# Kernel tuning notes

Measured on AMD Instinct MI355X. Metric: run time of the kernel, lower is better.

Reference implementation:

```python
import jax, jax.numpy as jnp
import numpy as np

INPUT_SIZE = 416
NUM_CLASSES = 80
A = 3  # anchors per yolo layer
SS = [13, 26, 52]  # grid sizes (strides 32/16/8)
ANCHORS = [[(116, 90), (156, 198), (373, 326)],
           [(30, 61), (62, 45), (59, 119)],
           [(10, 13), (16, 30), (33, 23)]]
B, L = 16, 50


def _build_priors():
    boxes, cols, rows, pws, phs, szs = [], [], [], [], [], []
    for l, S in enumerate(SS):
        for i in range(S):
            for j in range(S):
                cx, cy = (j + 0.5) / S, (i + 0.5) / S
                for (aw, ah) in ANCHORS[l]:
                    w, h = aw / INPUT_SIZE, ah / INPUT_SIZE
                    boxes.append((cx - 0.5 * w, cy - 0.5 * h, w, h))
                    cols.append(j); rows.append(i)
                    pws.append(aw); phs.append(ah); szs.append(S)
    f = lambda a: np.asarray(a, np.float32)
    return f(boxes), f(cols), f(rows), f(pws), f(phs), f(szs)

PRIORS_NP, PCOL_NP, PROW_NP, PPW_NP, PPH_NP, PS_NP = _build_priors()
N = PRIORS_NP.shape[0]  # 10647
OFF = np.concatenate([[0], np.cumsum([S * S * A for S in SS])])


def setup_inputs() -> dict:
    key = jax.random.key(0)
    ks = jax.random.split(key, 8)
    inp = {}
    for l, S in enumerate(SS):
        inp[f"yolo_out{l}"] = jax.random.normal(ks[l], (B, A * (NUM_CLASSES + 5), S, S), jnp.float32)
    cls = jax.random.randint(ks[3], (B, L), 0, NUM_CLASSES).astype(jnp.float32)
    valid = jax.random.uniform(ks[4], (B, L)) < 0.4
    cls = jnp.where(valid, cls, -1.0)  # class < 0 means padding label
    xy = jax.random.uniform(ks[5], (B, L, 2), minval=0.0, maxval=0.7)
    wh = jax.random.uniform(ks[6], (B, L, 2), minval=0.05, maxval=0.3)
    inp["labels"] = jnp.concatenate([cls[..., None], xy, wh], axis=-1)[:, None]  # [B,1,L,5]
    return inp


def _bce(p, t):
    # torch BCELoss (mean) with the same log clamp at -100
    lg = lambda x: jnp.maximum(jnp.log(x), -100.0)
    return jnp.mean(-(t * lg(p) + (1.0 - t) * lg(1.0 - p)))


def _build_targets(labels):
    pri = jnp.asarray(PRIORS_NP)
    lab = labels[:, 0]  # [B,L,5]
    cls = lab[..., 0]
    valid = cls >= 0.0  # [B,L]
    bx, by, bw, bh = lab[..., 1], lab[..., 2], lab[..., 3], lab[..., 4]
    px, py, pw, ph = pri[:, 0], pri[:, 1], pri[:, 2], pri[:, 3]
    # IoU of every label against every prior: [B,L,N]
    ix = jnp.maximum(px, bx[..., None]); iy = jnp.maximum(py, by[..., None])
    ax = jnp.minimum(px + pw, (bx + bw)[..., None]); ay = jnp.minimum(py + ph, (by + bh)[..., None])
    inter = jnp.maximum(ax - ix, 0.0) * jnp.maximum(ay - iy, 0.0)
    ious = inter / (pw * ph + (bw * bh)[..., None] - inter)

    # priors with IoU>=0.5 to any gt are ignored for objectness (unless chosen as best)
    suppressed = jnp.any((ious >= 0.5) & valid[..., None], axis=1)  # [B,N]

    # best prior per label; on ties, pick the middle tied index (as the original)
    m = jnp.max(ious, axis=-1, keepdims=True)
    tie = ious == m
    k = tie.sum(-1)
    rank = (k - 1) // 2 + 1
    cs = jnp.cumsum(tie, -1)
    idx = jnp.argmax(tie & (cs == rank[..., None]), axis=-1)  # [B,L]

    colc = jnp.asarray(PCOL_NP)[idx]; rowc = jnp.asarray(PROW_NP)[idx]
    pwc = jnp.asarray(PPW_NP)[idx]; phc = jnp.asarray(PPH_NP)[idx]
    Sc = jnp.asarray(PS_NP)[idx]
    dx = jnp.clip((bx + 0.5 * bw) * Sc - colc, 1e-6, 0.999999)
    dy = jnp.clip((by + 0.5 * bh) * Sc - rowc, 1e-6, 0.999999)
    t_all = jnp.stack([jnp.log(dx / (1.0 - dx)), jnp.log(dy / (1.0 - dy)),
                       jnp.log(bw * INPUT_SIZE / pwc), jnp.log(bh * INPUT_SIZE / phc)], -1)  # [B,L,4]

    flat = (jnp.arange(B)[:, None] * N + idx).reshape(-1)  # [B*L]
    vflat = valid.reshape(-1)
    g = jnp.arange(B * L)
    winner = jax.ops.segment_max(jnp.where(vflat, g, -1), flat, num_segments=B * N)
    chosen = winner >= 0  # [B*N]
    coord_t = jnp.where(chosen[:, None], t_all.reshape(-1, 4)[jnp.clip(winner, 0)], 0.0)

    cls_i = jnp.where(vflat, cls.reshape(-1).astype(jnp.int32), 0)
    class_t = jnp.zeros((B * N, NUM_CLASSES), jnp.float32).at[flat, cls_i].max(vflat.astype(jnp.float32))

    obj_t = chosen.astype(jnp.float32).reshape(B, N)
    obj_m = (chosen.reshape(B, N) | ~suppressed).astype(jnp.float32)
    pos_m = chosen.astype(jnp.float32).reshape(B, N)
    return jax.lax.stop_gradient(
        (obj_t, obj_m, pos_m, coord_t.reshape(B, N, 4), class_t.reshape(B, N, NUM_CLASSES)))


def reference(yolo_out0, yolo_out1, yolo_out2, labels):
    obj_t, obj_m, pos_m, coord_t, class_t = _build_targets(labels)
    outs = [yolo_out0, yolo_out1, yolo_out2]
    Cp5 = NUM_CLASSES + 5
    obj_loss = coord_loss = class_loss = 0.0
    for l, S in enumerate(SS):
        n0, n1 = int(OFF[l]), int(OFF[l + 1])
        out = outs[l]
        # per-prior ordering within a layer is (row, col, anchor)
        om = obj_m[:, n0:n1].reshape(B, S, S, A).transpose(0, 3, 1, 2)
        ot = obj_t[:, n0:n1].reshape(B, S, S, A).transpose(0, 3, 1, 2)
        pm = pos_m[:, n0:n1].reshape(B, S, S, A)
        ct = coord_t[:, n0:n1].reshape(B, S, S, A, 4).transpose(0, 3, 4, 1, 2).reshape(B, A * 4, S, S)
        cm = jnp.broadcast_to(pm[..., None], (B, S, S, A, 4)).transpose(0, 3, 4, 1, 2).reshape(B, A * 4, S, S)
        kt = class_t[:, n0:n1].reshape(B, S, S, A, NUM_CLASSES).transpose(0, 3, 4, 1, 2).reshape(B, A * NUM_CLASSES, S, S)
        km = jnp.broadcast_to(pm[..., None], (B, S, S, A, NUM_CLASSES)).transpose(0, 3, 4, 1, 2).reshape(B, A * NUM_CLASSES, S, S)
        oi = np.arange(A) * Cp5 + 4
        ci = (np.arange(A)[:, None] * Cp5 + np.arange(4)).reshape(-1)
        ki = (np.arange(A)[:, None] * Cp5 + 5 + np.arange(NUM_CLASSES)).reshape(-1)
        obj_loss = obj_loss + _bce(jax.nn.sigmoid(out[:, oi]) * om, ot * om)
        coord_loss = coord_loss + jnp.mean((out[:, ci] * cm - ct * cm) ** 2)
        class_loss = class_loss + _bce(jax.nn.sigmoid(out[:, ki]) * km, kt * km)
    return jnp.stack([obj_loss, coord_loss, class_loss])
```

## Files before the change

### kernel.cpp

```cpp
#include <hip/hip_runtime.h>

#define NPRI 10647
#define BB 16
#define LL 50
#define OBJ_BLOCKS 720
#define CHO_BLOCKS (BB * LL)
#define TOT_BLOCKS (OBJ_BLOCKS + CHO_BLOCKS)

#define SUPP_C 0.49999998509883880615234375

__device__ __constant__ double c_hw[3][3] = {
    {0.5*(116.0/416.0), 0.5*(156.0/416.0), 0.5*(373.0/416.0)},
    {0.5*( 30.0/416.0), 0.5*( 62.0/416.0), 0.5*( 59.0/416.0)},
    {0.5*( 10.0/416.0), 0.5*( 16.0/416.0), 0.5*( 33.0/416.0)}};
__device__ __constant__ double c_hh[3][3] = {
    {0.5*( 90.0/416.0), 0.5*(198.0/416.0), 0.5*(326.0/416.0)},
    {0.5*( 61.0/416.0), 0.5*( 45.0/416.0), 0.5*(119.0/416.0)},
    {0.5*( 23.0/416.0), 0.5*( 30.0/416.0), 0.5*( 23.0/416.0)}};
__device__ __constant__ float c_pwf[3][3] = {
    {(float)(116.0/416.0), (float)(156.0/416.0), (float)(373.0/416.0)},
    {(float)( 30.0/416.0), (float)( 62.0/416.0), (float)( 59.0/416.0)},
    {(float)( 10.0/416.0), (float)( 16.0/416.0), (float)( 33.0/416.0)}};
__device__ __constant__ float c_phf[3][3] = {
    {(float)( 90.0/416.0), (float)(198.0/416.0), (float)(326.0/416.0)},
    {(float)( 61.0/416.0), (float)( 45.0/416.0), (float)(119.0/416.0)},
    {(float)( 23.0/416.0), (float)( 30.0/416.0), (float)( 23.0/416.0)}};
__device__ __constant__ float c_pwph[3][3] = {
    {(float)(116.0/416.0)*(float)( 90.0/416.0), (float)(156.0/416.0)*(float)(198.0/416.0), (float)(373.0/416.0)*(float)(326.0/416.0)},
    {(float)( 30.0/416.0)*(float)( 61.0/416.0), (float)( 62.0/416.0)*(float)( 45.0/416.0), (float)( 59.0/416.0)*(float)(119.0/416.0)},
    {(float)( 10.0/416.0)*(float)( 23.0/416.0), (float)( 16.0/416.0)*(float)( 30.0/416.0), (float)( 33.0/416.0)*(float)( 23.0/416.0)}};
__device__ __constant__ float c_awf[3][3] = {{116,156,373},{30,62,59},{10,16,33}};
__device__ __constant__ float c_ahf[3][3] = {{90,198,326},{61,45,119},{23,30,23}};
__device__ __constant__ double c_wObj[3] = {1.0/8112.0, 1.0/32448.0, 1.0/129792.0};

__device__ inline void decode_prior(int n, int& level, int& S, int& ii, int& jj,
                                    int& aa, int& tb) {
    if (n < 507)        { level = 0; S = 13; int c = n / 3;            aa = n - 3*c;            jj = c % 13; ii = c / 13; tb = 0;   }
    else if (n < 2535)  { level = 1; S = 26; int nn = n - 507;  int c = nn / 3; aa = nn - 3*c; jj = c % 26; ii = c / 26; tb = 39;  }
    else                { level = 2; S = 52; int nn = n - 2535; int c = nn / 3; aa = nn - 3*c; jj = c % 52; ii = c / 52; tb = 117; }
}

__global__ __launch_bounds__(256) void assign_kernel(
    const float* __restrict__ labels, int* __restrict__ idxArr,
    float4* __restrict__ tcoord) {
    __shared__ float s_px[273], s_py[273], s_pxe[273], s_pye[273];
    __shared__ float s_iou[NPRI];
    __shared__ float s_w[4];
    __shared__ int   s_wsum[4];

    int tid = threadIdx.x, lane = tid & 63, wid = tid >> 6;
    int gi  = blockIdx.x;
    const float* lab = labels + gi * 5;
    float cls = lab[0];
    if (tid == 0) idxArr[gi] = -1;
    if (cls < 0.0f) return;

    for (int t = tid; t < 273; t += 256) {
        int level, aa, idx;
        if (t < 39)       { level = 0; aa = t / 13;           idx = t - 13 * aa; }
        else if (t < 117) { level = 1; int q = t - 39;  aa = q / 26; idx = q - 26 * aa; }
        else              { level = 2; int q = t - 117; aa = q / 52; idx = q - 52 * aa; }
        int S = (level == 0) ? 13 : (level == 1) ? 26 : 52;
        double c = ((double)idx + 0.5) / (double)S;
        float px = (float)(c - c_hw[level][aa]);
        float py = (float)(c - c_hh[level][aa]);
        s_px[t]  = px; s_pxe[t] = __fadd_rn(px, c_pwf[level][aa]);
        s_py[t]  = py; s_pye[t] = __fadd_rn(py, c_phf[level][aa]);
    }

    float bx = lab[1], by = lab[2], bw = lab[3], bh = lab[4];
    float bxe  = __fadd_rn(bx, bw), bye = __fadd_rn(by, bh);
    float bwbh = __fmul_rn(bw, bh);
    __syncthreads();

    float lmax = -3.0e38f;
    for (int n = tid; n < NPRI; n += 256) {
        int level, S, ii, jj, aa, tb;
        decode_prior(n, level, S, ii, jj, aa, tb);
        int tj = tb + aa * S + jj, ti = tb + aa * S + ii;
        float px = s_px[tj], pxe = s_pxe[tj];
        float py = s_py[ti], pye = s_pye[ti];
        float pwph = c_pwph[level][aa];
        float ix = fmaxf(px, bx), iy = fmaxf(py, by);
        float ax = fminf(pxe, bxe), ay = fminf(pye, bye);
        float iw = fmaxf(__fsub_rn(ax, ix), 0.0f);
        float ih = fmaxf(__fsub_rn(ay, iy), 0.0f);
        float inter = __fmul_rn(iw, ih);
        float denom = __fsub_rn(__fadd_rn(pwph, bwbh), inter);
        float iou = __fdiv_rn(inter, denom);
        s_iou[n] = iou;
        lmax = fmaxf(lmax, iou);
    }
    for (int d = 1; d < 64; d <<= 1) lmax = fmaxf(lmax, __shfl_xor(lmax, d));
    if (lane == 0) s_w[wid] = lmax;
    __syncthreads();
    float m = fmaxf(fmaxf(s_w[0], s_w[1]), fmaxf(s_w[2], s_w[3]));

    const int CH = 42;
    int start = tid * CH;
    int end   = min(start + CH, NPRI);
    int cnt = 0;
    for (int n = start; n < end; ++n) cnt += (s_iou[n] == m) ? 1 : 0;

    int incl = cnt;
    for (int d = 1; d < 64; d <<= 1) {
        int v = __shfl_up(incl, d);
        if (lane >= d) incl += v;
    }
    if (lane == 63) s_wsum[wid] = incl;
    __syncthreads();
    int woff = 0, k = 0;
    for (int w = 0; w < 4; ++w) { int v = s_wsum[w]; k += v; if (w < wid) woff += v; }
    int rank = (k - 1) / 2 + 1;
    int pre  = woff + incl - cnt;

    if (pre < rank && rank <= pre + cnt) {
        int r = rank - pre;
        int sel = -1;
        for (int n = start; n < end; ++n)
            if (s_iou[n] == m && --r == 0) { sel = n; break; }
        int level, S, ii, jj, aa, tb;
        decode_prior(sel, level, S, ii, jj, aa, tb);
        float Sf = (float)S, colf = (float)jj, rowf = (float)ii;
        float dx = __fsub_rn(__fmul_rn(__fadd_rn(bx, __fmul_rn(0.5f, bw)), Sf), colf);
        float dy = __fsub_rn(__fmul_rn(__fadd_rn(by, __fmul_rn(0.5f, bh)), Sf), rowf);
        dx = fminf(fmaxf(dx, 1e-6f), 0.999999f);
        dy = fminf(fmaxf(dy, 1e-6f), 0.999999f);
        float t0 = logf(__fdiv_rn(dx, __fsub_rn(1.0f, dx)));
        float t1 = logf(__fdiv_rn(dy, __fsub_rn(1.0f, dy)));
        float t2 = logf(__fdiv_rn(__fmul_rn(bw, 416.0f), c_awf[level][aa]));
        float t3 = logf(__fdiv_rn(__fmul_rn(bh, 416.0f), c_ahf[level][aa]));
        tcoord[gi] = make_float4(t0, t1, t2, t3);
        idxArr[gi] = sel;
    }
}

__global__ __launch_bounds__(256) void loss_kernel(
    const float* __restrict__ o0, const float* __restrict__ o1, const float* __restrict__ o2,
    const float* __restrict__ labels, const int* __restrict__ idxArr,
    const float4* __restrict__ tcoord,
    double* __restrict__ pObj, double* __restrict__ pCoord, double* __restrict__ pClass) {
    __shared__ float  s_pxv[52], s_pyv[52], s_pxev[52], s_pyev[52];
    __shared__ float  s_lbx[LL], s_lby[LL], s_lxe[LL], s_lye[LL], s_lar[LL];
    __shared__ int    s_lidx[LL];
    __shared__ int    s_lcnt;
    __shared__ int    s_cidx[LL];
    __shared__ float  s_ccls[LL];
    __shared__ double s_red[256];
    int tid = threadIdx.x, lane = tid & 63, wid = tid >> 6;

    if (blockIdx.x < OBJ_BLOCKS) {
        int bid = blockIdx.x;
        int level, m, chunk, S, SS2, lvloff;
        if (bid < 48)       { level = 0; m = bid;         chunk = 0;           S = 13; SS2 = 169;  lvloff = 0;    }
        else if (bid < 192) { level = 1; int q = bid-48;  m = q / 3;  chunk = q - 3*m;  S = 26; SS2 = 676;  lvloff = 507;  }
        else                { level = 2; int q = bid-192; m = q / 11; chunk = q - 11*m; S = 52; SS2 = 2704; lvloff = 2535; }
        int b  = m / 3;
        int aa = m - 3 * b;
        int pos = chunk * 256 + tid;

        if (tid < S) {
            double c = ((double)tid + 0.5) / (double)S;
            float px = (float)(c - c_hw[level][aa]);
            float py = (float)(c - c_hh[level][aa]);
            s_pxv[tid]  = px; s_pxev[tid] = __fadd_rn(px, c_pwf[level][aa]);
            s_pyv[tid]  = py; s_pyev[tid] = __fadd_rn(py, c_phf[level][aa]);
        }
        if (wid == 0) {
            float cls = -1.0f, lbx = 0, lby = 0, lbw = 0, lbh = 0; int idx = -1;
            if (lane < LL) {
                const float* lab = labels + (b * LL + lane) * 5;
                cls = lab[0]; lbx = lab[1]; lby = lab[2]; lbw = lab[3]; lbh = lab[4];
                idx = idxArr[b * LL + lane];
            }
            bool valid = (lane < LL) && (cls >= 0.0f);
            unsigned long long mask = __ballot(valid);
            if (valid) {
                int p = __popcll(mask & ((1ull << lane) - 1ull));
                s_lbx[p] = lbx;
                s_lby[p] = lby;
                s_lxe[p] = __fadd_rn(lbx, lbw);
                s_lye[p] = __fadd_rn(lby, lbh);
                s_lar[p] = __fmul_rn(lbw, lbh);
                s_lidx[p] = idx;
            }
            if (lane == 0) s_lcnt = __popcll(mask);
        }
        __syncthreads();

        double a = 0.0;
        if (pos < SS2) {
            const float* outp = (level == 0) ? o0 : ((level == 1) ? o1 : o2);
            float x = outp[((size_t)b * 255 + aa * 85 + 4) * SS2 + pos];
            int ii = pos / S, jj = pos - ii * S;
            int n  = lvloff + pos * 3 + aa;
            float px = s_pxv[jj], pxe = s_pxev[jj];
            float py = s_pyv[ii], pye = s_pyev[ii];
            float pwph = c_pwph[level][aa];
            bool supp = false, chosen = false;
            int cnt = s_lcnt;
            for (int l = 0; l < cnt; ++l) {
                chosen = chosen | (s_lidx[l] == n);
                float ix = fmaxf(px, s_lbx[l]);
                float iy = fmaxf(py, s_lby[l]);
                float ax = fminf(pxe, s_lxe[l]);
                float ay = fminf(pye, s_lye[l]);
                float iw = fmaxf(__fsub_rn(ax, ix), 0.0f);
                float ih = fmaxf(__fsub_rn(ay, iy), 0.0f);
                float inter = __fmul_rn(iw, ih);
                float denom = __fsub_rn(__fadd_rn(pwph, s_lar[l]), inter);
                supp = supp | ((double)inter >= SUPP_C * (double)denom);
            }
            if (chosen || !supp) {
                float p = 1.0f / (1.0f + expf(-x));
                float t = chosen ? 1.0f : 0.0f;
                float lp = fmaxf(logf(p), -100.0f);
                float lq = fmaxf(logf(1.0f - p), -100.0f);
                a = -(double)(t * lp + (1.0f - t) * lq) * c_wObj[level];
            }
        }
        s_red[tid] = a; __syncthreads();
        for (int s = 128; s > 0; s >>= 1) { if (tid < s) s_red[tid] += s_red[tid + s]; __syncthreads(); }
        if (tid == 0) pObj[bid] = s_red[0];
    } else {
        int gi = blockIdx.x - OBJ_BLOCKS;
        int b  = gi / LL, lsel = gi - b * LL;
        if (tid < LL) {
            s_cidx[tid] = idxArr[b * LL + tid];
            s_ccls[tid] = labels[(b * LL + tid) * 5];
        }
        __syncthreads();
        int sel = s_cidx[lsel];
        int maxl = -1;
        if (sel >= 0)
            for (int l = 0; l < LL; ++l) if (s_cidx[l] == sel) maxl = l;
        bool active = (sel >= 0) && (maxl == lsel);

        double vc = 0.0, vk = 0.0;
        if (active) {
            int level, S, ii, jj, aa, tb;
            decode_prior(sel, level, S, ii, jj, aa, tb);
            int SS2 = S * S;
            const float* outp = (level == 0) ? o0 : ((level == 1) ? o1 : o2);
            const float* base = outp + (size_t)b * 255 * SS2 + aa * 85 * SS2 + ii * S + jj;
            double wObj = c_wObj[level];
            if (tid < 4) {
                float4 ct = tcoord[gi];
                float ctk = (tid == 0) ? ct.x : (tid == 1) ? ct.y : (tid == 2) ? ct.z : ct.w;
                float x = base[tid * SS2];
                float d = __fsub_rn(x, ctk);
                vc = (double)__fmul_rn(d, d) * (wObj * 0.25);
            } else if (tid >= 5 && tid < 85) {
                int cc = tid - 5;
                float x = base[tid * SS2];
                float t = 0.0f;
                for (int l = 0; l < LL; ++l)
                    if (s_cidx[l] == sel && (int)s_ccls[l] == cc) t = 1.0f;
                float p = 1.0f / (1.0f + expf(-x));
                float lp = fmaxf(logf(p), -100.0f);
                float lq = fmaxf(logf(1.0f - p), -100.0f);
                vk = -(double)(t * lp + (1.0f - t) * lq) * (wObj * 0.0125);
            }
        }
        s_red[tid] = vc; __syncthreads();
        for (int s = 128; s > 0; s >>= 1) { if (tid < s) s_red[tid] += s_red[tid + s]; __syncthreads(); }
        if (tid == 0) pCoord[gi] = s_red[0];
        __syncthreads();
        s_red[tid] = vk; __syncthreads();
        for (int s = 128; s > 0; s >>= 1) { if (tid < s) s_red[tid] += s_red[tid + s]; __syncthreads(); }
        if (tid == 0) pClass[gi] = s_red[0];
    }
}

__global__ __launch_bounds__(256) void finalize_kernel(
    const double* __restrict__ pObj, const double* __restrict__ pCoord,
    const double* __restrict__ pClass, float* __restrict__ out) {
    int tid = threadIdx.x;
    double sO = 0.0, sC = 0.0, sK = 0.0;
    for (int i = tid; i < OBJ_BLOCKS; i += 256) sO += pObj[i];
    for (int i = tid; i < CHO_BLOCKS; i += 256) { sC += pCoord[i]; sK += pClass[i]; }
    __shared__ double r0[256], r1[256], r2[256];
    r0[tid] = sO; r1[tid] = sC; r2[tid] = sK;
    __syncthreads();
    for (int s = 128; s > 0; s >>= 1) {
        if (tid < s) { r0[tid] += r0[tid + s]; r1[tid] += r1[tid + s]; r2[tid] += r2[tid + s]; }
        __syncthreads();
    }
    if (tid == 0) { out[0] = (float)r0[0]; out[1] = (float)r1[0]; out[2] = (float)r2[0]; }
}

extern "C" void kernel_launch(void* const* d_in, const int* in_sizes, int n_in,
                              void* d_out, int out_size, void* d_ws, size_t ws_size,
                              hipStream_t stream) {
    const float* o0     = (const float*)d_in[0];
    const float* o1     = (const float*)d_in[1];
    const float* o2     = (const float*)d_in[2];
    const float* labels = (const float*)d_in[3];

    char* ws = (char*)d_ws;
    int*    idxArr = (int*)   (ws);
    float4* tcoord = (float4*)(ws + 3200);
    double* pObj   = (double*)(ws + 16000);
    double* pCoord = (double*)(ws + 21760);
    double* pClass = (double*)(ws + 28160);

    assign_kernel<<<BB * LL, 256, 0, stream>>>(labels, idxArr, tcoord);
    loss_kernel<<<TOT_BLOCKS, 256, 0, stream>>>(o0, o1, o2, labels, idxArr, tcoord,
                                                pObj, pCoord, pClass);
    finalize_kernel<<<1, 256, 0, stream>>>(pObj, pCoord, pClass, (float*)d_out);
}
```

Before: 122.3 us.

## Fuse assign, loss and finalize kernels into one cooperative kernel with grid syncs

Merges the three launches into a single cooperative kernel of 800 blocks that uses grid-wide syncs between the assignment, loss and final-reduction phases. The per-label IoU array is no longer kept in shared memory; IoU values are recomputed in the max, count and select passes so that shared memory per block shrinks and more blocks can be resident. The aim is to remove launch overhead and inter-kernel gaps, at the cost of extra IoU arithmetic, grid-sync cost, and the loss blocks doing both objectness and class work serially.

```diff
diff --git a/kernel.cpp b/kernel.cpp
--- a/kernel.cpp
+++ b/kernel.cpp
@@ -1,11 +1,14 @@
 #include <hip/hip_runtime.h>
+#include <hip/hip_cooperative_groups.h>
+
+namespace cg = cooperative_groups;
 
 #define NPRI 10647
 #define BB 16
 #define LL 50
 #define OBJ_BLOCKS 720
 #define CHO_BLOCKS (BB * LL)
-#define TOT_BLOCKS (OBJ_BLOCKS + CHO_BLOCKS)
+#define GRID_BLOCKS CHO_BLOCKS
 
 #define SUPP_C 0.49999998509883880615234375
 
@@ -40,106 +43,15 @@
     else                { level = 2; S = 52; int nn = n - 2535; int c = nn / 3; aa = nn - 3*c; jj = c % 52; ii = c / 52; tb = 117; }
 }
 
-__global__ __launch_bounds__(256) void assign_kernel(
-    const float* __restrict__ labels, int* __restrict__ idxArr,
-    float4* __restrict__ tcoord) {
-    __shared__ float s_px[273], s_py[273], s_pxe[273], s_pye[273];
-    __shared__ float s_iou[NPRI];
-    __shared__ float s_w[4];
-    __shared__ int   s_wsum[4];
-
-    int tid = threadIdx.x, lane = tid & 63, wid = tid >> 6;
-    int gi  = blockIdx.x;
-    const float* lab = labels + gi * 5;
-    float cls = lab[0];
-    if (tid == 0) idxArr[gi] = -1;
-    if (cls < 0.0f) return;
-
-    for (int t = tid; t < 273; t += 256) {
-        int level, aa, idx;
-        if (t < 39)       { level = 0; aa = t / 13;           idx = t - 13 * aa; }
-        else if (t < 117) { level = 1; int q = t - 39;  aa = q / 26; idx = q - 26 * aa; }
-        else              { level = 2; int q = t - 117; aa = q / 52; idx = q - 52 * aa; }
-        int S = (level == 0) ? 13 : (level == 1) ? 26 : 52;
-        double c = ((double)idx + 0.5) / (double)S;
-        float px = (float)(c - c_hw[level][aa]);
-        float py = (float)(c - c_hh[level][aa]);
-        s_px[t]  = px; s_pxe[t] = __fadd_rn(px, c_pwf[level][aa]);
-        s_py[t]  = py; s_pye[t] = __fadd_rn(py, c_phf[level][aa]);
-    }
-
-    float bx = lab[1], by = lab[2], bw = lab[3], bh = lab[4];
-    float bxe  = __fadd_rn(bx, bw), bye = __fadd_rn(by, bh);
-    float bwbh = __fmul_rn(bw, bh);
-    __syncthreads();
-
-    float lmax = -3.0e38f;
-    for (int n = tid; n < NPRI; n += 256) {
-        int level, S, ii, jj, aa, tb;
-        decode_prior(n, level, S, ii, jj, aa, tb);
-        int tj = tb + aa * S + jj, ti = tb + aa * S + ii;
-        float px = s_px[tj], pxe = s_pxe[tj];
-        float py = s_py[ti], pye = s_pye[ti];
-        float pwph = c_pwph[level][aa];
-        float ix = fmaxf(px, bx), iy = fmaxf(py, by);
-        float ax = fminf(pxe, bxe), ay = fminf(pye, bye);
-        float iw = fmaxf(__fsub_rn(ax, ix), 0.0f);
-        float ih = fmaxf(__fsub_rn(ay, iy), 0.0f);
-        float inter = __fmul_rn(iw, ih);
-        float denom = __fsub_rn(__fadd_rn(pwph, bwbh), inter);
-        float iou = __fdiv_rn(inter, denom);
-        s_iou[n] = iou;
-        lmax = fmaxf(lmax, iou);
-    }
-    for (int d = 1; d < 64; d <<= 1) lmax = fmaxf(lmax, __shfl_xor(lmax, d));
-    if (lane == 0) s_w[wid] = lmax;
-    __syncthreads();
-    float m = fmaxf(fmaxf(s_w[0], s_w[1]), fmaxf(s_w[2], s_w[3]));
-
-    const int CH = 42;
-    int start = tid * CH;
-    int end   = min(start + CH, NPRI);
-    int cnt = 0;
-    for (int n = start; n < end; ++n) cnt += (s_iou[n] == m) ? 1 : 0;
-
-    int incl = cnt;
-    for (int d = 1; d < 64; d <<= 1) {
-        int v = __shfl_up(incl, d);
-        if (lane >= d) incl += v;
-    }
-    if (lane == 63) s_wsum[wid] = incl;
-    __syncthreads();
-    int woff = 0, k = 0;
-    for (int w = 0; w < 4; ++w) { int v = s_wsum[w]; k += v; if (w < wid) woff += v; }
-    int rank = (k - 1) / 2 + 1;
-    int pre  = woff + incl - cnt;
-
-    if (pre < rank && rank <= pre + cnt) {
-        int r = rank - pre;
-        int sel = -1;
-        for (int n = start; n < end; ++n)
-            if (s_iou[n] == m && --r == 0) { sel = n; break; }
-        int level, S, ii, jj, aa, tb;
-        decode_prior(sel, level, S, ii, jj, aa, tb);
-        float Sf = (float)S, colf = (float)jj, rowf = (float)ii;
-        float dx = __fsub_rn(__fmul_rn(__fadd_rn(bx, __fmul_rn(0.5f, bw)), Sf), colf);
-        float dy = __fsub_rn(__fmul_rn(__fadd_rn(by, __fmul_rn(0.5f, bh)), Sf), rowf);
-        dx = fminf(fmaxf(dx, 1e-6f), 0.999999f);
-        dy = fminf(fmaxf(dy, 1e-6f), 0.999999f);
-        float t0 = logf(__fdiv_rn(dx, __fsub_rn(1.0f, dx)));
-        float t1 = logf(__fdiv_rn(dy, __fsub_rn(1.0f, dy)));
-        float t2 = logf(__fdiv_rn(__fmul_rn(bw, 416.0f), c_awf[level][aa]));
-        float t3 = logf(__fdiv_rn(__fmul_rn(bh, 416.0f), c_ahf[level][aa]));
-        tcoord[gi] = make_float4(t0, t1, t2, t3);
-        idxArr[gi] = sel;
-    }
-}
-
-__global__ __launch_bounds__(256) void loss_kernel(
-    const float* __restrict__ o0, const float* __restrict__ o1, const float* __restrict__ o2,
-    const float* __restrict__ labels, const int* __restrict__ idxArr,
-    const float4* __restrict__ tcoord,
-    double* __restrict__ pObj, double* __restrict__ pCoord, double* __restrict__ pClass) {
+__global__ __launch_bounds__(256, 4) void yolo_fused(
+    const float* __restrict__ o0, const float* __restrict__ o1,
+    const float* __restrict__ o2, const float* __restrict__ labels,
+    int* __restrict__ idxArr, float4* __restrict__ tcoord,
+    double* __restrict__ pObj, double* __restrict__ pCoord,
+    double* __restrict__ pClass, float* __restrict__ out) {
+    __shared__ float  s_px[273], s_py[273], s_pxe[273], s_pye[273];
+    __shared__ float  s_w[4];
+    __shared__ int    s_wsum[4];
     __shared__ float  s_pxv[52], s_pyv[52], s_pxev[52], s_pyev[52];
     __shared__ float  s_lbx[LL], s_lby[LL], s_lxe[LL], s_lye[LL], s_lar[LL];
     __shared__ int    s_lidx[LL];
@@ -147,16 +59,103 @@
     __shared__ int    s_cidx[LL];
     __shared__ float  s_ccls[LL];
     __shared__ double s_red[256];
+
     int tid = threadIdx.x, lane = tid & 63, wid = tid >> 6;
-
-    if (blockIdx.x < OBJ_BLOCKS) {
-        int bid = blockIdx.x;
-        int level, m, chunk, S, SS2, lvloff;
-        if (bid < 48)       { level = 0; m = bid;         chunk = 0;           S = 13; SS2 = 169;  lvloff = 0;    }
-        else if (bid < 192) { level = 1; int q = bid-48;  m = q / 3;  chunk = q - 3*m;  S = 26; SS2 = 676;  lvloff = 507;  }
-        else                { level = 2; int q = bid-192; m = q / 11; chunk = q - 11*m; S = 52; SS2 = 2704; lvloff = 2535; }
-        int b  = m / 3;
-        int aa = m - 3 * b;
+    int gi  = blockIdx.x;
+
+    {
+        const float* lab = labels + gi * 5;
+        float cls = lab[0];
+        if (tid == 0) idxArr[gi] = -1;
+        if (cls >= 0.0f) {
+            for (int t = tid; t < 273; t += 256) {
+                int level, aa, idx;
+                if (t < 39)       { level = 0; aa = t / 13;           idx = t - 13 * aa; }
+                else if (t < 117) { level = 1; int q = t - 39;  aa = q / 26; idx = q - 26 * aa; }
+                else              { level = 2; int q = t - 117; aa = q / 52; idx = q - 52 * aa; }
+                int S = (level == 0) ? 13 : (level == 1) ? 26 : 52;
+                double c = ((double)idx + 0.5) / (double)S;
+                float px = (float)(c - c_hw[level][aa]);
+                float py = (float)(c - c_hh[level][aa]);
+                s_px[t]  = px; s_pxe[t] = __fadd_rn(px, c_pwf[level][aa]);
+                s_py[t]  = py; s_pye[t] = __fadd_rn(py, c_phf[level][aa]);
+            }
+            float bx = lab[1], by = lab[2], bw = lab[3], bh = lab[4];
+            float bxe  = __fadd_rn(bx, bw), bye = __fadd_rn(by, bh);
+            float bwbh = __fmul_rn(bw, bh);
+            __syncthreads();
+
+            auto iou_of = [&](int n) -> float {
+                int level, S, ii, jj, aa, tb;
+                decode_prior(n, level, S, ii, jj, aa, tb);
+                int tj = tb + aa * S + jj, ti = tb + aa * S + ii;
+                float px = s_px[tj], pxe = s_pxe[tj];
+                float py = s_py[ti], pye = s_pye[ti];
+                float ix = fmaxf(px, bx), iy = fmaxf(py, by);
+                float ax = fminf(pxe, bxe), ay = fminf(pye, bye);
+                float iw = fmaxf(__fsub_rn(ax, ix), 0.0f);
+                float ih = fmaxf(__fsub_rn(ay, iy), 0.0f);
+                float inter = __fmul_rn(iw, ih);
+                float denom = __fsub_rn(__fadd_rn(c_pwph[level][aa], bwbh), inter);
+                return __fdiv_rn(inter, denom);
+            };
+
+            float lmax = -3.0e38f;
+            for (int n = tid; n < NPRI; n += 256) lmax = fmaxf(lmax, iou_of(n));
+            for (int d = 1; d < 64; d <<= 1) lmax = fmaxf(lmax, __shfl_xor(lmax, d));
+            if (lane == 0) s_w[wid] = lmax;
+            __syncthreads();
+            float m = fmaxf(fmaxf(s_w[0], s_w[1]), fmaxf(s_w[2], s_w[3]));
+
+            const int CH = 42;
+            int start = tid * CH;
+            int end   = min(start + CH, NPRI);
+            int cnt = 0;
+            for (int n = start; n < end; ++n) cnt += (iou_of(n) == m) ? 1 : 0;
+
+            int incl = cnt;
+            for (int d = 1; d < 64; d <<= 1) {
+                int v = __shfl_up(incl, d);
+                if (lane >= d) incl += v;
+            }
+            if (lane == 63) s_wsum[wid] = incl;
+            __syncthreads();
+            int woff = 0, k = 0;
+            for (int w = 0; w < 4; ++w) { int v = s_wsum[w]; k += v; if (w < wid) woff += v; }
+            int rank = (k - 1) / 2 + 1;
+            int pre  = woff + incl - cnt;
+
+            if (pre < rank && rank <= pre + cnt) {
+                int r = rank - pre;
+                int sel = -1;
+                for (int n = start; n < end; ++n)
+                    if (iou_of(n) == m && --r == 0) { sel = n; break; }
+                int level, S, ii, jj, aa, tb;
+                decode_prior(sel, level, S, ii, jj, aa, tb);
+                float Sf = (float)S, colf = (float)jj, rowf = (float)ii;
+                float dx = __fsub_rn(__fmul_rn(__fadd_rn(bx, __fmul_rn(0.5f, bw)), Sf), colf);
+                float dy = __fsub_rn(__fmul_rn(__fadd_rn(by, __fmul_rn(0.5f, bh)), Sf), rowf);
+                dx = fminf(fmaxf(dx, 1e-6f), 0.999999f);
+                dy = fminf(fmaxf(dy, 1e-6f), 0.999999f);
+                float t0 = logf(__fdiv_rn(dx, __fsub_rn(1.0f, dx)));
+                float t1 = logf(__fdiv_rn(dy, __fsub_rn(1.0f, dy)));
+                float t2 = logf(__fdiv_rn(__fmul_rn(bw, 416.0f), c_awf[level][aa]));
+                float t3 = logf(__fdiv_rn(__fmul_rn(bh, 416.0f), c_ahf[level][aa]));
+                tcoord[gi] = make_float4(t0, t1, t2, t3);
+                idxArr[gi] = sel;
+            }
+        }
+    }
+
+    cg::this_grid().sync();
+
+    if (gi < OBJ_BLOCKS) {
+        int level, mi, chunk, S, SS2, lvloff;
+        if (gi < 48)       { level = 0; mi = gi;          chunk = 0;            S = 13; SS2 = 169;  lvloff = 0;    }
+        else if (gi < 192) { level = 1; int q = gi - 48;  mi = q / 3;  chunk = q - 3 * mi;  S = 26; SS2 = 676;  lvloff = 507;  }
+        else               { level = 2; int q = gi - 192; mi = q / 11; chunk = q - 11 * mi; S = 52; SS2 = 2704; lvloff = 2535; }
+        int b  = mi / 3;
+        int aa = mi - 3 * b;
         int pos = chunk * 256 + tid;
 
         if (tid < S) {
@@ -221,10 +220,12 @@
         }
         s_red[tid] = a; __syncthreads();
         for (int s = 128; s > 0; s >>= 1) { if (tid < s) s_red[tid] += s_red[tid + s]; __syncthreads(); }
-        if (tid == 0) pObj[bid] = s_red[0];
-    } else {
-        int gi = blockIdx.x - OBJ_BLOCKS;
-        int b  = gi / LL, lsel = gi - b * LL;
+        if (tid == 0) pObj[gi] = s_red[0];
+    }
+    __syncthreads();
+
+    {
+        int b = gi / LL, lsel = gi - b * LL;
         if (tid < LL) {
             s_cidx[tid] = idxArr[b * LL + tid];
             s_ccls[tid] = labels[(b * LL + tid) * 5];
@@ -270,23 +271,26 @@
         for (int s = 128; s > 0; s >>= 1) { if (tid < s) s_red[tid] += s_red[tid + s]; __syncthreads(); }
         if (tid == 0) pClass[gi] = s_red[0];
     }
-}
-
-__global__ __launch_bounds__(256) void finalize_kernel(
-    const double* __restrict__ pObj, const double* __restrict__ pCoord,
-    const double* __restrict__ pClass, float* __restrict__ out) {
-    int tid = threadIdx.x;
-    double sO = 0.0, sC = 0.0, sK = 0.0;
-    for (int i = tid; i < OBJ_BLOCKS; i += 256) sO += pObj[i];
-    for (int i = tid; i < CHO_BLOCKS; i += 256) { sC += pCoord[i]; sK += pClass[i]; }
-    __shared__ double r0[256], r1[256], r2[256];
-    r0[tid] = sO; r1[tid] = sC; r2[tid] = sK;
-    __syncthreads();
-    for (int s = 128; s > 0; s >>= 1) {
-        if (tid < s) { r0[tid] += r0[tid + s]; r1[tid] += r1[tid + s]; r2[tid] += r2[tid + s]; }
-        __syncthreads();
+
+    cg::this_grid().sync();
+
+    if (gi == 0) {
+        double sO = 0.0, sC = 0.0, sK = 0.0;
+        for (int i = tid; i < OBJ_BLOCKS; i += 256) sO += pObj[i];
+        for (int i = tid; i < CHO_BLOCKS; i += 256) { sC += pCoord[i]; sK += pClass[i]; }
+        __syncthreads();
+        s_red[tid] = sO; __syncthreads();
+        for (int s = 128; s > 0; s >>= 1) { if (tid < s) s_red[tid] += s_red[tid + s]; __syncthreads(); }
+        if (tid == 0) out[0] = (float)s_red[0];
+        __syncthreads();
+        s_red[tid] = sC; __syncthreads();
+        for (int s = 128; s > 0; s >>= 1) { if (tid < s) s_red[tid] += s_red[tid + s]; __syncthreads(); }
+        if (tid == 0) out[1] = (float)s_red[0];
+        __syncthreads();
+        s_red[tid] = sK; __syncthreads();
+        for (int s = 128; s > 0; s >>= 1) { if (tid < s) s_red[tid] += s_red[tid + s]; __syncthreads(); }
+        if (tid == 0) out[2] = (float)s_red[0];
     }
-    if (tid == 0) { out[0] = (float)r0[0]; out[1] = (float)r1[0]; out[2] = (float)r2[0]; }
 }
 
 extern "C" void kernel_launch(void* const* d_in, const int* in_sizes, int n_in,
@@ -303,9 +307,11 @@
     double* pObj   = (double*)(ws + 16000);
     double* pCoord = (double*)(ws + 21760);
     double* pClass = (double*)(ws + 28160);
-
-    assign_kernel<<<BB * LL, 256, 0, stream>>>(labels, idxArr, tcoord);
-    loss_kernel<<<TOT_BLOCKS, 256, 0, stream>>>(o0, o1, o2, labels, idxArr, tcoord,
-                                                pObj, pCoord, pClass);
-    finalize_kernel<<<1, 256, 0, stream>>>(pObj, pCoord, pClass, (float*)d_out);
+    float*  outp   = (float*)d_out;
+
+    void* args[] = {(void*)&o0, (void*)&o1, (void*)&o2, (void*)&labels,
+                    (void*)&idxArr, (void*)&tcoord,
+                    (void*)&pObj, (void*)&pCoord, (void*)&pClass, (void*)&outp};
+    hipLaunchCooperativeKernel((const void*)yolo_fused, dim3(GRID_BLOCKS), dim3(256),
+                               args, 0, stream);
 }
```

Measured after the change: 325.2 us. 2.66x slower.

## Decouple objectness loss from assignment and apply chosen-prior correction separately

Applied to the files above, without the earlier changes.

The objectness loss pass no longer depends on the per-label prior assignment. It is merged into the same launch as the assignment blocks, so the two run concurrently instead of one after the other. Chosen priors are handled later in the chosen-prior kernel through a correction term: it adds the positive-target BCE and subtracts the negative term if one had been counted. The prior coordinate table is also precomputed at compile time into constant memory, replacing the per-block double-precision setup. The cost is a larger shared-memory footprint for the merged kernel, which may lower occupancy for the objectness blocks, plus one extra partial-sum array.

```diff
diff --git a/kernel.cpp b/kernel.cpp
--- a/kernel.cpp
+++ b/kernel.cpp
@@ -3,28 +3,49 @@
 #define NPRI 10647
 #define BB 16
 #define LL 50
+#define ASS_BLOCKS (BB * LL)
 #define OBJ_BLOCKS 720
+#define A_BLOCKS (ASS_BLOCKS + OBJ_BLOCKS)
 #define CHO_BLOCKS (BB * LL)
-#define TOT_BLOCKS (OBJ_BLOCKS + CHO_BLOCKS)
 
 #define SUPP_C 0.49999998509883880615234375
 
-__device__ __constant__ double c_hw[3][3] = {
+constexpr double HWd[3][3] = {
     {0.5*(116.0/416.0), 0.5*(156.0/416.0), 0.5*(373.0/416.0)},
     {0.5*( 30.0/416.0), 0.5*( 62.0/416.0), 0.5*( 59.0/416.0)},
     {0.5*( 10.0/416.0), 0.5*( 16.0/416.0), 0.5*( 33.0/416.0)}};
-__device__ __constant__ double c_hh[3][3] = {
+constexpr double HHd[3][3] = {
     {0.5*( 90.0/416.0), 0.5*(198.0/416.0), 0.5*(326.0/416.0)},
     {0.5*( 61.0/416.0), 0.5*( 45.0/416.0), 0.5*(119.0/416.0)},
     {0.5*( 23.0/416.0), 0.5*( 30.0/416.0), 0.5*( 23.0/416.0)}};
-__device__ __constant__ float c_pwf[3][3] = {
+constexpr float PWf[3][3] = {
     {(float)(116.0/416.0), (float)(156.0/416.0), (float)(373.0/416.0)},
     {(float)( 30.0/416.0), (float)( 62.0/416.0), (float)( 59.0/416.0)},
     {(float)( 10.0/416.0), (float)( 16.0/416.0), (float)( 33.0/416.0)}};
-__device__ __constant__ float c_phf[3][3] = {
+constexpr float PHf[3][3] = {
     {(float)( 90.0/416.0), (float)(198.0/416.0), (float)(326.0/416.0)},
     {(float)( 61.0/416.0), (float)( 45.0/416.0), (float)(119.0/416.0)},
     {(float)( 23.0/416.0), (float)( 30.0/416.0), (float)( 23.0/416.0)}};
+
+struct PTab { float px[273], pxe[273], py[273], pye[273]; };
+constexpr PTab make_ptab() {
+    PTab t{};
+    for (int tt = 0; tt < 273; ++tt) {
+        int level, aa, idx;
+        if (tt < 39)       { level = 0; aa = tt / 13;           idx = tt - 13 * aa; }
+        else if (tt < 117) { level = 1; int q = tt - 39;  aa = q / 26; idx = q - 26 * aa; }
+        else               { level = 2; int q = tt - 117; aa = q / 52; idx = q - 52 * aa; }
+        int S = (level == 0) ? 13 : (level == 1) ? 26 : 52;
+        double c = ((double)idx + 0.5) / (double)S;
+        float px = (float)(c - HWd[level][aa]);
+        float py = (float)(c - HHd[level][aa]);
+        t.px[tt] = px; t.pxe[tt] = px + PWf[level][aa];
+        t.py[tt] = py; t.pye[tt] = py + PHf[level][aa];
+    }
+    return t;
+}
+__device__ __constant__ PTab g_ptab = make_ptab();
+
 __device__ __constant__ float c_pwph[3][3] = {
     {(float)(116.0/416.0)*(float)( 90.0/416.0), (float)(156.0/416.0)*(float)(198.0/416.0), (float)(373.0/416.0)*(float)(326.0/416.0)},
     {(float)( 30.0/416.0)*(float)( 61.0/416.0), (float)( 62.0/416.0)*(float)( 45.0/416.0), (float)( 59.0/416.0)*(float)(119.0/416.0)},
@@ -40,138 +61,117 @@
     else                { level = 2; S = 52; int nn = n - 2535; int c = nn / 3; aa = nn - 3*c; jj = c % 52; ii = c / 52; tb = 117; }
 }
 
-__global__ __launch_bounds__(256) void assign_kernel(
-    const float* __restrict__ labels, int* __restrict__ idxArr,
-    float4* __restrict__ tcoord) {
+__global__ __launch_bounds__(256) void assign_obj_kernel(
+    const float* __restrict__ o0, const float* __restrict__ o1,
+    const float* __restrict__ o2, const float* __restrict__ labels,
+    int* __restrict__ idxArr, float4* __restrict__ tcoord,
+    double* __restrict__ pObj) {
     __shared__ float s_px[273], s_py[273], s_pxe[273], s_pye[273];
     __shared__ float s_iou[NPRI];
     __shared__ float s_w[4];
     __shared__ int   s_wsum[4];
+    __shared__ float s_lbx[LL], s_lby[LL], s_lxe[LL], s_lye[LL], s_lar[LL];
+    __shared__ int   s_lcnt;
+    __shared__ double s_red[256];
 
     int tid = threadIdx.x, lane = tid & 63, wid = tid >> 6;
     int gi  = blockIdx.x;
-    const float* lab = labels + gi * 5;
-    float cls = lab[0];
-    if (tid == 0) idxArr[gi] = -1;
-    if (cls < 0.0f) return;
-
-    for (int t = tid; t < 273; t += 256) {
-        int level, aa, idx;
-        if (t < 39)       { level = 0; aa = t / 13;           idx = t - 13 * aa; }
-        else if (t < 117) { level = 1; int q = t - 39;  aa = q / 26; idx = q - 26 * aa; }
-        else              { level = 2; int q = t - 117; aa = q / 52; idx = q - 52 * aa; }
-        int S = (level == 0) ? 13 : (level == 1) ? 26 : 52;
-        double c = ((double)idx + 0.5) / (double)S;
-        float px = (float)(c - c_hw[level][aa]);
-        float py = (float)(c - c_hh[level][aa]);
-        s_px[t]  = px; s_pxe[t] = __fadd_rn(px, c_pwf[level][aa]);
-        s_py[t]  = py; s_pye[t] = __fadd_rn(py, c_phf[level][aa]);
-    }
-
-    float bx = lab[1], by = lab[2], bw = lab[3], bh = lab[4];
-    float bxe  = __fadd_rn(bx, bw), bye = __fadd_rn(by, bh);
-    float bwbh = __fmul_rn(bw, bh);
-    __syncthreads();
-
-    float lmax = -3.0e38f;
-    for (int n = tid; n < NPRI; n += 256) {
-        int level, S, ii, jj, aa, tb;
-        decode_prior(n, level, S, ii, jj, aa, tb);
-        int tj = tb + aa * S + jj, ti = tb + aa * S + ii;
-        float px = s_px[tj], pxe = s_pxe[tj];
-        float py = s_py[ti], pye = s_pye[ti];
-        float pwph = c_pwph[level][aa];
-        float ix = fmaxf(px, bx), iy = fmaxf(py, by);
-        float ax = fminf(pxe, bxe), ay = fminf(pye, bye);
-        float iw = fmaxf(__fsub_rn(ax, ix), 0.0f);
-        float ih = fmaxf(__fsub_rn(ay, iy), 0.0f);
-        float inter = __fmul_rn(iw, ih);
-        float denom = __fsub_rn(__fadd_rn(pwph, bwbh), inter);
-        float iou = __fdiv_rn(inter, denom);
-        s_iou[n] = iou;
-        lmax = fmaxf(lmax, iou);
-    }
-    for (int d = 1; d < 64; d <<= 1) lmax = fmaxf(lmax, __shfl_xor(lmax, d));
-    if (lane == 0) s_w[wid] = lmax;
-    __syncthreads();
-    float m = fmaxf(fmaxf(s_w[0], s_w[1]), fmaxf(s_w[2], s_w[3]));
-
-    const int CH = 42;
-    int start = tid * CH;
-    int end   = min(start + CH, NPRI);
-    int cnt = 0;
-    for (int n = start; n < end; ++n) cnt += (s_iou[n] == m) ? 1 : 0;
-
-    int incl = cnt;
-    for (int d = 1; d < 64; d <<= 1) {
-        int v = __shfl_up(incl, d);
-        if (lane >= d) incl += v;
-    }
-    if (lane == 63) s_wsum[wid] = incl;
-    __syncthreads();
-    int woff = 0, k = 0;
-    for (int w = 0; w < 4; ++w) { int v = s_wsum[w]; k += v; if (w < wid) woff += v; }
-    int rank = (k - 1) / 2 + 1;
-    int pre  = woff + incl - cnt;
-
-    if (pre < rank && rank <= pre + cnt) {
-        int r = rank - pre;
-        int sel = -1;
-        for (int n = start; n < end; ++n)
-            if (s_iou[n] == m && --r == 0) { sel = n; break; }
-        int level, S, ii, jj, aa, tb;
-        decode_prior(sel, level, S, ii, jj, aa, tb);
-        float Sf = (float)S, colf = (float)jj, rowf = (float)ii;
-        float dx = __fsub_rn(__fmul_rn(__fadd_rn(bx, __fmul_rn(0.5f, bw)), Sf), colf);
-        float dy = __fsub_rn(__fmul_rn(__fadd_rn(by, __fmul_rn(0.5f, bh)), Sf), rowf);
-        dx = fminf(fmaxf(dx, 1e-6f), 0.999999f);
-        dy = fminf(fmaxf(dy, 1e-6f), 0.999999f);
-        float t0 = logf(__fdiv_rn(dx, __fsub_rn(1.0f, dx)));
-        float t1 = logf(__fdiv_rn(dy, __fsub_rn(1.0f, dy)));
-        float t2 = logf(__fdiv_rn(__fmul_rn(bw, 416.0f), c_awf[level][aa]));
-        float t3 = logf(__fdiv_rn(__fmul_rn(bh, 416.0f), c_ahf[level][aa]));
-        tcoord[gi] = make_float4(t0, t1, t2, t3);
-        idxArr[gi] = sel;
-    }
-}
-
-__global__ __launch_bounds__(256) void loss_kernel(
-    const float* __restrict__ o0, const float* __restrict__ o1, const float* __restrict__ o2,
-    const float* __restrict__ labels, const int* __restrict__ idxArr,
-    const float4* __restrict__ tcoord,
-    double* __restrict__ pObj, double* __restrict__ pCoord, double* __restrict__ pClass) {
-    __shared__ float  s_pxv[52], s_pyv[52], s_pxev[52], s_pyev[52];
-    __shared__ float  s_lbx[LL], s_lby[LL], s_lxe[LL], s_lye[LL], s_lar[LL];
-    __shared__ int    s_lidx[LL];
-    __shared__ int    s_lcnt;
-    __shared__ int    s_cidx[LL];
-    __shared__ float  s_ccls[LL];
-    __shared__ double s_red[256];
-    int tid = threadIdx.x, lane = tid & 63, wid = tid >> 6;
-
-    if (blockIdx.x < OBJ_BLOCKS) {
-        int bid = blockIdx.x;
-        int level, m, chunk, S, SS2, lvloff;
-        if (bid < 48)       { level = 0; m = bid;         chunk = 0;           S = 13; SS2 = 169;  lvloff = 0;    }
-        else if (bid < 192) { level = 1; int q = bid-48;  m = q / 3;  chunk = q - 3*m;  S = 26; SS2 = 676;  lvloff = 507;  }
-        else                { level = 2; int q = bid-192; m = q / 11; chunk = q - 11*m; S = 52; SS2 = 2704; lvloff = 2535; }
+
+    if (gi < ASS_BLOCKS) {
+        const float* lab = labels + gi * 5;
+        float cls = lab[0];
+        if (tid == 0) idxArr[gi] = -1;
+        if (cls < 0.0f) return;
+
+        for (int t = tid; t < 273; t += 256) {
+            s_px[t] = g_ptab.px[t]; s_pxe[t] = g_ptab.pxe[t];
+            s_py[t] = g_ptab.py[t]; s_pye[t] = g_ptab.pye[t];
+        }
+        float bx = lab[1], by = lab[2], bw = lab[3], bh = lab[4];
+        float bxe  = __fadd_rn(bx, bw), bye = __fadd_rn(by, bh);
+        float bwbh = __fmul_rn(bw, bh);
+        __syncthreads();
+
+        float lmax = -3.0e38f;
+        for (int n = tid; n < NPRI; n += 256) {
+            int level, S, ii, jj, aa, tb;
+            decode_prior(n, level, S, ii, jj, aa, tb);
+            int tj = tb + aa * S + jj, ti = tb + aa * S + ii;
+            float px = s_px[tj], pxe = s_pxe[tj];
+            float py = s_py[ti], pye = s_pye[ti];
+            float pwph = c_pwph[level][aa];
+            float ix = fmaxf(px, bx), iy = fmaxf(py, by);
+            float ax = fminf(pxe, bxe), ay = fminf(pye, bye);
+            float iw = fmaxf(__fsub_rn(ax, ix), 0.0f);
+            float ih = fmaxf(__fsub_rn(ay, iy), 0.0f);
+            float inter = __fmul_rn(iw, ih);
+            float denom = __fsub_rn(__fadd_rn(pwph, bwbh), inter);
+            float iou = __fdiv_rn(inter, denom);
+            s_iou[n] = iou;
+            lmax = fmaxf(lmax, iou);
+        }
+        for (int d = 1; d < 64; d <<= 1) lmax = fmaxf(lmax, __shfl_xor(lmax, d));
+        if (lane == 0) s_w[wid] = lmax;
+        __syncthreads();
+        float m = fmaxf(fmaxf(s_w[0], s_w[1]), fmaxf(s_w[2], s_w[3]));
+
+        const int CH = 42;
+        int start = tid * CH;
+        int end   = min(start + CH, NPRI);
+        int cnt = 0;
+        for (int n = start; n < end; ++n) cnt += (s_iou[n] == m) ? 1 : 0;
+
+        int incl = cnt;
+        for (int d = 1; d < 64; d <<= 1) {
+            int v = __shfl_up(incl, d);
+            if (lane >= d) incl += v;
+        }
+        if (lane == 63) s_wsum[wid] = incl;
+        __syncthreads();
+        int woff = 0, k = 0;
+        for (int w = 0; w < 4; ++w) { int v = s_wsum[w]; k += v; if (w < wid) woff += v; }
+        int rank = (k - 1) / 2 + 1;
+        int pre  = woff + incl - cnt;
+
+        if (pre < rank && rank <= pre + cnt) {
+            int r = rank - pre;
+            int sel = -1;
+            for (int n = start; n < end; ++n)
+                if (s_iou[n] == m && --r == 0) { sel = n; break; }
+            int level, S, ii, jj, aa, tb;
+            decode_prior(sel, level, S, ii, jj, aa, tb);
+            float Sf = (float)S, colf = (float)jj, rowf = (float)ii;
+            float dx = __fsub_rn(__fmul_rn(__fadd_rn(bx, __fmul_rn(0.5f, bw)), Sf), colf);
+            float dy = __fsub_rn(__fmul_rn(__fadd_rn(by, __fmul_rn(0.5f, bh)), Sf), rowf);
+            dx = fminf(fmaxf(dx, 1e-6f), 0.999999f);
+            dy = fminf(fmaxf(dy, 1e-6f), 0.999999f);
+            float t0 = logf(__fdiv_rn(dx, __fsub_rn(1.0f, dx)));
+            float t1 = logf(__fdiv_rn(dy, __fsub_rn(1.0f, dy)));
+            float t2 = logf(__fdiv_rn(__fmul_rn(bw, 416.0f), c_awf[level][aa]));
+            float t3 = logf(__fdiv_rn(__fmul_rn(bh, 416.0f), c_ahf[level][aa]));
+            tcoord[gi] = make_float4(t0, t1, t2, t3);
+            idxArr[gi] = sel;
+        }
+    } else {
+        int bid = gi - ASS_BLOCKS;
+        int level, m, chunk, S, SS2;
+        if (bid < 48)       { level = 0; m = bid;         chunk = 0;           S = 13; SS2 = 169;  }
+        else if (bid < 192) { level = 1; int q = bid-48;  m = q / 3;  chunk = q - 3*m;  S = 26; SS2 = 676;  }
+        else                { level = 2; int q = bid-192; m = q / 11; chunk = q - 11*m; S = 52; SS2 = 2704; }
         int b  = m / 3;
         int aa = m - 3 * b;
         int pos = chunk * 256 + tid;
 
         if (tid < S) {
-            double c = ((double)tid + 0.5) / (double)S;
-            float px = (float)(c - c_hw[level][aa]);
-            float py = (float)(c - c_hh[level][aa]);
-            s_pxv[tid]  = px; s_pxev[tid] = __fadd_rn(px, c_pwf[level][aa]);
-            s_pyv[tid]  = py; s_pyev[tid] = __fadd_rn(py, c_phf[level][aa]);
+            int tb = ((level == 0) ? 0 : (level == 1) ? 39 : 117) + aa * S;
+            s_px[tid]  = g_ptab.px[tb + tid];  s_pxe[tid] = g_ptab.pxe[tb + tid];
+            s_py[tid]  = g_ptab.py[tb + tid];  s_pye[tid] = g_ptab.pye[tb + tid];
         }
         if (wid == 0) {
-            float cls = -1.0f, lbx = 0, lby = 0, lbw = 0, lbh = 0; int idx = -1;
+            float cls = -1.0f, lbx = 0, lby = 0, lbw = 0, lbh = 0;
             if (lane < LL) {
                 const float* lab = labels + (b * LL + lane) * 5;
                 cls = lab[0]; lbx = lab[1]; lby = lab[2]; lbw = lab[3]; lbh = lab[4];
-                idx = idxArr[b * LL + lane];
             }
             bool valid = (lane < LL) && (cls >= 0.0f);
             unsigned long long mask = __ballot(valid);
@@ -182,7 +182,6 @@
                 s_lxe[p] = __fadd_rn(lbx, lbw);
                 s_lye[p] = __fadd_rn(lby, lbh);
                 s_lar[p] = __fmul_rn(lbw, lbh);
-                s_lidx[p] = idx;
             }
             if (lane == 0) s_lcnt = __popcll(mask);
         }
@@ -193,14 +192,12 @@
             const float* outp = (level == 0) ? o0 : ((level == 1) ? o1 : o2);
             float x = outp[((size_t)b * 255 + aa * 85 + 4) * SS2 + pos];
             int ii = pos / S, jj = pos - ii * S;
-            int n  = lvloff + pos * 3 + aa;
-            float px = s_pxv[jj], pxe = s_pxev[jj];
-            float py = s_pyv[ii], pye = s_pyev[ii];
+            float px = s_px[jj], pxe = s_pxe[jj];
+            float py = s_py[ii], pye = s_pye[ii];
             float pwph = c_pwph[level][aa];
-            bool supp = false, chosen = false;
+            bool supp = false;
             int cnt = s_lcnt;
             for (int l = 0; l < cnt; ++l) {
-                chosen = chosen | (s_lidx[l] == n);
                 float ix = fmaxf(px, s_lbx[l]);
                 float iy = fmaxf(py, s_lby[l]);
                 float ax = fminf(pxe, s_lxe[l]);
@@ -211,74 +208,118 @@
                 float denom = __fsub_rn(__fadd_rn(pwph, s_lar[l]), inter);
                 supp = supp | ((double)inter >= SUPP_C * (double)denom);
             }
-            if (chosen || !supp) {
+            if (!supp) {
                 float p = 1.0f / (1.0f + expf(-x));
-                float t = chosen ? 1.0f : 0.0f;
-                float lp = fmaxf(logf(p), -100.0f);
                 float lq = fmaxf(logf(1.0f - p), -100.0f);
-                a = -(double)(t * lp + (1.0f - t) * lq) * c_wObj[level];
+                a = -(double)lq * c_wObj[level];
             }
         }
         s_red[tid] = a; __syncthreads();
         for (int s = 128; s > 0; s >>= 1) { if (tid < s) s_red[tid] += s_red[tid + s]; __syncthreads(); }
         if (tid == 0) pObj[bid] = s_red[0];
-    } else {
-        int gi = blockIdx.x - OBJ_BLOCKS;
-        int b  = gi / LL, lsel = gi - b * LL;
-        if (tid < LL) {
-            s_cidx[tid] = idxArr[b * LL + tid];
-            s_ccls[tid] = labels[(b * LL + tid) * 5];
-        }
-        __syncthreads();
-        int sel = s_cidx[lsel];
-        int maxl = -1;
-        if (sel >= 0)
-            for (int l = 0; l < LL; ++l) if (s_cidx[l] == sel) maxl = l;
-        bool active = (sel >= 0) && (maxl == lsel);
-
-        double vc = 0.0, vk = 0.0;
-        if (active) {
-            int level, S, ii, jj, aa, tb;
-            decode_prior(sel, level, S, ii, jj, aa, tb);
-            int SS2 = S * S;
-            const float* outp = (level == 0) ? o0 : ((level == 1) ? o1 : o2);
-            const float* base = outp + (size_t)b * 255 * SS2 + aa * 85 * SS2 + ii * S + jj;
-            double wObj = c_wObj[level];
-            if (tid < 4) {
-                float4 ct = tcoord[gi];
-                float ctk = (tid == 0) ? ct.x : (tid == 1) ? ct.y : (tid == 2) ? ct.z : ct.w;
-                float x = base[tid * SS2];
-                float d = __fsub_rn(x, ctk);
-                vc = (double)__fmul_rn(d, d) * (wObj * 0.25);
-            } else if (tid >= 5 && tid < 85) {
-                int cc = tid - 5;
-                float x = base[tid * SS2];
-                float t = 0.0f;
-                for (int l = 0; l < LL; ++l)
-                    if (s_cidx[l] == sel && (int)s_ccls[l] == cc) t = 1.0f;
+    }
+}
+
+__global__ __launch_bounds__(256) void cho_kernel(
+    const float* __restrict__ o0, const float* __restrict__ o1,
+    const float* __restrict__ o2, const float* __restrict__ labels,
+    const int* __restrict__ idxArr, const float4* __restrict__ tcoord,
+    double* __restrict__ pCoord, double* __restrict__ pClass,
+    double* __restrict__ pCorr) {
+    __shared__ int    s_cidx[LL];
+    __shared__ float  s_ccls[LL];
+    __shared__ double s_red[256];
+    int tid = threadIdx.x, lane = tid & 63, wid = tid >> 6;
+    int gi = blockIdx.x;
+    int b  = gi / LL, lsel = gi - b * LL;
+
+    if (tid < LL) {
+        s_cidx[tid] = idxArr[b * LL + tid];
+        s_ccls[tid] = labels[(b * LL + tid) * 5];
+    }
+    __syncthreads();
+    int sel = s_cidx[lsel];
+    int maxl = -1;
+    if (sel >= 0)
+        for (int l = 0; l < LL; ++l) if (s_cidx[l] == sel) maxl = l;
+    bool active = (sel >= 0) && (maxl == lsel);
+
+    double vc = 0.0, vk = 0.0, vcorr = 0.0;
+    if (active) {
+        int level, S, ii, jj, aa, tb;
+        decode_prior(sel, level, S, ii, jj, aa, tb);
+        int SS2 = S * S;
+        const float* outp = (level == 0) ? o0 : ((level == 1) ? o1 : o2);
+        const float* base = outp + (size_t)b * 255 * SS2 + aa * 85 * SS2 + ii * S + jj;
+        double wObj = c_wObj[level];
+        if (tid < 4) {
+            float4 ct = tcoord[gi];
+            float ctk = (tid == 0) ? ct.x : (tid == 1) ? ct.y : (tid == 2) ? ct.z : ct.w;
+            float x = base[tid * SS2];
+            float d = __fsub_rn(x, ctk);
+            vc = (double)__fmul_rn(d, d) * (wObj * 0.25);
+        } else if (tid >= 5 && tid < 85) {
+            int cc = tid - 5;
+            float x = base[tid * SS2];
+            float t = 0.0f;
+            for (int l = 0; l < LL; ++l)
+                if (s_cidx[l] == sel && (int)s_ccls[l] == cc) t = 1.0f;
+            float p = 1.0f / (1.0f + expf(-x));
+            float lp = fmaxf(logf(p), -100.0f);
+            float lq = fmaxf(logf(1.0f - p), -100.0f);
+            vk = -(double)(t * lp + (1.0f - t) * lq) * (wObj * 0.0125);
+        }
+        if (wid == 0) {
+            int tj = tb + aa * S + jj, ti = tb + aa * S + ii;
+            float px = g_ptab.px[tj], pxe = g_ptab.pxe[tj];
+            float py = g_ptab.py[ti], pye = g_ptab.pye[ti];
+            float pwph = c_pwph[level][aa];
+            bool vote = false;
+            if (lane < LL) {
+                const float* lab = labels + (b * LL + lane) * 5;
+                if (lab[0] >= 0.0f) {
+                    float lbx = lab[1], lby = lab[2], lbw = lab[3], lbh = lab[4];
+                    float lxe = __fadd_rn(lbx, lbw), lye = __fadd_rn(lby, lbh);
+                    float lar = __fmul_rn(lbw, lbh);
+                    float ix = fmaxf(px, lbx);
+                    float iy = fmaxf(py, lby);
+                    float ax = fminf(pxe, lxe);
+                    float ay = fminf(pye, lye);
+                    float iw = fmaxf(__fsub_rn(ax, ix), 0.0f);
+                    float ih = fmaxf(__fsub_rn(ay, iy), 0.0f);
+                    float inter = __fmul_rn(iw, ih);
+                    float denom = __fsub_rn(__fadd_rn(pwph, lar), inter);
+                    vote = ((double)inter >= SUPP_C * (double)denom);
+                }
+            }
+            unsigned long long bal = __ballot(vote);
+            if (lane == 0) {
+                bool supp = (bal != 0ull);
+                float x = base[4 * SS2];
                 float p = 1.0f / (1.0f + expf(-x));
                 float lp = fmaxf(logf(p), -100.0f);
                 float lq = fmaxf(logf(1.0f - p), -100.0f);
-                vk = -(double)(t * lp + (1.0f - t) * lq) * (wObj * 0.0125);
-            }
-        }
-        s_red[tid] = vc; __syncthreads();
-        for (int s = 128; s > 0; s >>= 1) { if (tid < s) s_red[tid] += s_red[tid + s]; __syncthreads(); }
-        if (tid == 0) pCoord[gi] = s_red[0];
-        __syncthreads();
-        s_red[tid] = vk; __syncthreads();
-        for (int s = 128; s > 0; s >>= 1) { if (tid < s) s_red[tid] += s_red[tid + s]; __syncthreads(); }
-        if (tid == 0) pClass[gi] = s_red[0];
-    }
+                vcorr = -(double)lp * wObj - (supp ? 0.0 : -(double)lq * wObj);
+            }
+        }
+    }
+    s_red[tid] = vc; __syncthreads();
+    for (int s = 128; s > 0; s >>= 1) { if (tid < s) s_red[tid] += s_red[tid + s]; __syncthreads(); }
+    if (tid == 0) pCoord[gi] = s_red[0];
+    __syncthreads();
+    s_red[tid] = vk; __syncthreads();
+    for (int s = 128; s > 0; s >>= 1) { if (tid < s) s_red[tid] += s_red[tid + s]; __syncthreads(); }
+    if (tid == 0) { pClass[gi] = s_red[0]; pCorr[gi] = vcorr; }
 }
 
 __global__ __launch_bounds__(256) void finalize_kernel(
-    const double* __restrict__ pObj, const double* __restrict__ pCoord,
-    const double* __restrict__ pClass, float* __restrict__ out) {
+    const double* __restrict__ pObj, const double* __restrict__ pCorr,
+    const double* __restrict__ pCoord, const double* __restrict__ pClass,
+    float* __restrict__ out) {
     int tid = threadIdx.x;
     double sO = 0.0, sC = 0.0, sK = 0.0;
     for (int i = tid; i < OBJ_BLOCKS; i += 256) sO += pObj[i];
-    for (int i = tid; i < CHO_BLOCKS; i += 256) { sC += pCoord[i]; sK += pClass[i]; }
+    for (int i = tid; i < CHO_BLOCKS; i += 256) { sO += pCorr[i]; sC += pCoord[i]; sK += pClass[i]; }
     __shared__ double r0[256], r1[256], r2[256];
     r0[tid] = sO; r1[tid] = sC; r2[tid] = sK;
     __syncthreads();
@@ -303,9 +344,12 @@
     double* pObj   = (double*)(ws + 16000);
     double* pCoord = (double*)(ws + 21760);
     double* pClass = (double*)(ws + 28160);
-
-    assign_kernel<<<BB * LL, 256, 0, stream>>>(labels, idxArr, tcoord);
-    loss_kernel<<<TOT_BLOCKS, 256, 0, stream>>>(o0, o1, o2, labels, idxArr, tcoord,
-                                                pObj, pCoord, pClass);
-    finalize_kernel<<<1, 256, 0, stream>>>(pObj, pCoord, pClass, (float*)d_out);
-}
+    double* pCorr  = (double*)(ws + 34560);
+
+    assign_obj_kernel<<<A_BLOCKS, 256, 0, stream>>>(o0, o1, o2, labels,
+                                                    idxArr, tcoord, pObj);
+    cho_kernel<<<CHO_BLOCKS, 256, 0, stream>>>(o0, o1, o2, labels, idxArr, tcoord,
+                                               pCoord, pClass, pCorr);
+    finalize_kernel<<<1, 256, 0, stream>>>(pObj, pCorr, pCoord, pClass,
+                                           (float*)d_out);
+}
```

After: 120.3 us, median of 2. About the same (-1.7%).
